# Optimization experiments

Hardware: AMD Instinct MI355X
Metric: run time of the kernel (lower is better)

Reference implementation:

```python
import jax, jax.numpy as jnp
import numpy as np

B, D, N, K = 4, 256, 4096, 8192


def setup_inputs() -> dict:
    key = jax.random.key(0)
    kx, ke = jax.random.split(key)
    x = jax.random.normal(kx, (B, D, N), dtype=jnp.float32)
    e = jax.random.normal(ke, (K, D), dtype=jnp.float32)
    return {"x": x, "e": e}


def reference(x, e):
    # encode: cdist(x^T [B,N,D], e [K,D]) -> [B,N,K]; argmin over K.
    # sqrt is monotonic, so argmin of squared distance == argmin of cdist.
    xt = jnp.transpose(x, (0, 2, 1))                      # [B,N,D]
    x2 = jnp.sum(xt * xt, axis=-1, keepdims=True)         # [B,N,1]
    e2 = jnp.sum(e * e, axis=-1)                          # [K]
    d2 = x2 - 2.0 * jnp.einsum('bnd,kd->bnk', xt, e) + e2 # [B,N,K]
    codes = jnp.argmin(d2, axis=-1)                       # [B,N]
    # decode: embedding gather then transpose back to [B,D,N]
    quantized = e[codes]                                  # [B,N,D]
    return jnp.transpose(quantized, (0, 2, 1))            # [B,D,N]
```

## Files before the change

kernel.cpp:

```cpp
#include <hip/hip_runtime.h>
#include <stdint.h>

#define B_ 4
#define D_ 256
#define N_ 4096
#define K_ 8192
#define Q_ (B_*N_)

#define KSPLIT_ 4
#define KSLICE_ (K_/KSPLIT_)
#define CHUNK_ 64
#define NCHUNK_ (KSLICE_/CHUNK_)
#define QTILE_ 256

typedef __attribute__((ext_vector_type(8))) short bf16x8;
typedef __attribute__((ext_vector_type(16))) float f32x16;

__device__ __forceinline__ unsigned short f32_to_bf16(float f) {
  unsigned u = __float_as_uint(f);
  unsigned r = 0x7FFFu + ((u >> 16) & 1u);
  return (unsigned short)((u + r) >> 16);
}
__device__ __forceinline__ float bf16_to_f32(unsigned short h) {
  return __uint_as_float(((unsigned)h) << 16);
}

__device__ __forceinline__ void gl_lds16(const void* g, void* l) {
  __builtin_amdgcn_global_load_lds(
      (const __attribute__((address_space(1))) unsigned int*)g,
      (__attribute__((address_space(3))) unsigned int*)l, 16, 0, 0);
}

__global__ void prep_x_kernel(const float* __restrict__ x,
                              unsigned short* __restrict__ xh,
                              unsigned short* __restrict__ xl) {
  __shared__ float tile[32][33];
  int b = blockIdx.z;
  int d0 = blockIdx.y * 32;
  int n0 = blockIdx.x * 32;
  int tx = threadIdx.x, ty = threadIdx.y;
  const float* xp = x + ((size_t)b * D_ + d0) * N_ + n0;
#pragma unroll
  for (int i = 0; i < 4; ++i)
    tile[ty + 8 * i][tx] = xp[(size_t)(ty + 8 * i) * N_ + tx];
  __syncthreads();
#pragma unroll
  for (int i = 0; i < 4; ++i) {
    int nl = ty + 8 * i;
    float v = -tile[tx][nl];
    unsigned short h = f32_to_bf16(v);
    unsigned short l = f32_to_bf16(v - bf16_to_f32(h));
    size_t q = (size_t)b * N_ + n0 + nl;
    xh[q * D_ + d0 + tx] = h;
    xl[q * D_ + d0 + tx] = l;
  }
}

__global__ void prep_e_kernel(const float* __restrict__ e,
                              unsigned short* __restrict__ eh,
                              unsigned short* __restrict__ el,
                              float* __restrict__ e2h,
                              unsigned long long* __restrict__ keys) {
  int k = blockIdx.x;
  int d = threadIdx.x;
  if (d < 2) keys[(size_t)k * 2 + d] = ~0ull;
  float v = e[(size_t)k * D_ + d];
  unsigned short h = f32_to_bf16(v);
  unsigned short l = f32_to_bf16(v - bf16_to_f32(h));
  eh[(size_t)k * D_ + d] = h;
  el[(size_t)k * D_ + d] = l;
  float s = v * v;
#pragma unroll
  for (int off = 32; off > 0; off >>= 1) s += __shfl_down(s, off, 64);
  __shared__ float ws4[4];
  if ((threadIdx.x & 63) == 0) ws4[threadIdx.x >> 6] = s;
  __syncthreads();
  if (threadIdx.x == 0) e2h[k] = 0.5f * (ws4[0] + ws4[1] + ws4[2] + ws4[3]);
}

__global__ __launch_bounds__(512, 2) void vq_main_kernel(
    const unsigned short* __restrict__ xh, const unsigned short* __restrict__ xl,
    const unsigned short* __restrict__ eh, const unsigned short* __restrict__ el,
    const float* __restrict__ e2h, unsigned long long* __restrict__ keys) {
  __shared__ __attribute__((aligned(16))) unsigned short Bs[2][2][CHUNK_ * 256];

  const int tid = threadIdx.x;
  const int w = tid >> 6;
  const int lane = tid & 63;
  const int l = lane & 31;
  const int hi = lane >> 5;

  const int qt = blockIdx.x >> 2;
  const int ksl = blockIdx.x & 3;
  const int q0 = qt * QTILE_;
  const int kbase = ksl * KSLICE_;
  const int qw = q0 + w * 32;

  bf16x8 ah[16], al[16];
  {
    const unsigned short* pa = xh + (size_t)(qw + l) * D_ + hi * 8;
    const unsigned short* pb = xl + (size_t)(qw + l) * D_ + hi * 8;
#pragma unroll
    for (int kc16 = 0; kc16 < 16; ++kc16) {
      ah[kc16] = *(const bf16x8*)(pa + kc16 * 16);
      al[kc16] = *(const bf16x8*)(pb + kc16 * 16);
    }
  }

  float rminv[16];
  int rmini[16];
#pragma unroll
  for (int r = 0; r < 16; ++r) { rminv[r] = __builtin_inff(); rmini[r] = 0; }

  auto stage = [&](int ch, int buf) {
    const int kc = kbase + ch * CHUNK_;
#pragma unroll
    for (int p = 0; p < 4; ++p) {
      const int c0 = w * 8 + p * 2;
      const int c = c0 + hi;
      const int g = l ^ (c & 31);
      const size_t srcoff = (size_t)(kc + c) * D_ + g * 8;
      gl_lds16(eh + srcoff, &Bs[buf][0][c0 * 256]);
      gl_lds16(el + srcoff, &Bs[buf][1][c0 * 256]);
    }
  };

  stage(0, 0);

#pragma unroll 1
  for (int ch = 0; ch < NCHUNK_; ++ch) {
    const int buf = ch & 1;
    __syncthreads();
    if (ch + 1 < NCHUNK_) stage(ch + 1, buf ^ 1);
    const int kc = kbase + ch * CHUNK_;
    const float e2v0 = e2h[kc + l];
    const float e2v1 = e2h[kc + 32 + l];

    {
      f32x16 acc;
#pragma unroll
      for (int r = 0; r < 16; ++r) acc[r] = e2v0;
#pragma unroll
      for (int ks = 0; ks < 16; ++ks) {
        const int pos = (((ks * 2 + hi) ^ l) * 8);
        bf16x8 bh = *(const bf16x8*)&Bs[buf][0][l * 256 + pos];
        bf16x8 bl = *(const bf16x8*)&Bs[buf][1][l * 256 + pos];
        acc = __builtin_amdgcn_mfma_f32_32x32x16_bf16(ah[ks], bh, acc, 0, 0, 0);
        acc = __builtin_amdgcn_mfma_f32_32x32x16_bf16(ah[ks], bl, acc, 0, 0, 0);
        acc = __builtin_amdgcn_mfma_f32_32x32x16_bf16(al[ks], bh, acc, 0, 0, 0);
      }
      const int kidx = kc + l;
#pragma unroll
      for (int r = 0; r < 16; ++r) {
        bool better = acc[r] < rminv[r];
        rminv[r] = better ? acc[r] : rminv[r];
        rmini[r] = better ? kidx : rmini[r];
      }
    }

    {
      f32x16 acc;
#pragma unroll
      for (int r = 0; r < 16; ++r) acc[r] = e2v1;
#pragma unroll
      for (int ks = 0; ks < 16; ++ks) {
        const int pos = (((ks * 2 + hi) ^ l) * 8);
        bf16x8 bh = *(const bf16x8*)&Bs[buf][0][(32 + l) * 256 + pos];
        bf16x8 bl = *(const bf16x8*)&Bs[buf][1][(32 + l) * 256 + pos];
        acc = __builtin_amdgcn_mfma_f32_32x32x16_bf16(ah[ks], bh, acc, 0, 0, 0);
        acc = __builtin_amdgcn_mfma_f32_32x32x16_bf16(ah[ks], bl, acc, 0, 0, 0);
        acc = __builtin_amdgcn_mfma_f32_32x32x16_bf16(al[ks], bh, acc, 0, 0, 0);
      }
      const int kidx = kc + 32 + l;
#pragma unroll
      for (int r = 0; r < 16; ++r) {
        bool better = acc[r] < rminv[r];
        rminv[r] = better ? acc[r] : rminv[r];
        rmini[r] = better ? kidx : rmini[r];
      }
    }
  }

#pragma unroll
  for (int r = 0; r < 16; ++r) {
    float bv = rminv[r];
    int bi = rmini[r];
#pragma unroll
    for (int xm = 1; xm <= 16; xm <<= 1) {
      float ov = __shfl_xor(bv, xm, 64);
      int oi = __shfl_xor(bi, xm, 64);
      if (ov < bv || (ov == bv && oi < bi)) { bv = ov; bi = oi; }
    }
    if (l == 0) {
      const int m = (r & 3) + 8 * (r >> 2) + 4 * hi;
      const int qq = qw + m;
      unsigned su = __float_as_uint(bv);
      su ^= (unsigned)(((int)su >> 31) | 0x80000000u);
      unsigned long long key = ((unsigned long long)su << 32) | (unsigned)bi;
      atomicMin(keys + qq, key);
    }
  }
}

__global__ void decode_kernel(const unsigned long long* __restrict__ keys,
                              const float* __restrict__ e,
                              float* __restrict__ out) {
  __shared__ float tile[32][33];
  __shared__ int codes[32];
  int b = blockIdx.y;
  int n0 = blockIdx.x * 32;
  int tx = threadIdx.x, ty = threadIdx.y;
  if (ty == 0)
    codes[tx] = (int)(keys[(size_t)b * N_ + n0 + tx] & 0xFFFFFFFFull);
  __syncthreads();
#pragma unroll 1
  for (int d0 = 0; d0 < D_; d0 += 32) {
#pragma unroll
    for (int i = 0; i < 4; ++i) {
      int nl = ty + 8 * i;
      tile[nl][tx] = e[(size_t)codes[nl] * D_ + d0 + tx];
    }
    __syncthreads();
#pragma unroll
    for (int i = 0; i < 4; ++i) {
      int dl = ty + 8 * i;
      out[((size_t)b * D_ + d0 + dl) * N_ + n0 + tx] = tile[tx][dl];
    }
    __syncthreads();
  }
}

extern "C" void kernel_launch(void* const* d_in, const int* in_sizes, int n_in,
                              void* d_out, int out_size, void* d_ws, size_t ws_size,
                              hipStream_t stream) {
  const float* x = (const float*)d_in[0];
  const float* e = (const float*)d_in[1];
  float* out = (float*)d_out;

  char* wksp = (char*)d_ws;
  unsigned short* xh = (unsigned short*)wksp;
  unsigned short* xl = xh + (size_t)Q_ * D_;
  unsigned short* eh = xl + (size_t)Q_ * D_;
  unsigned short* el = eh + (size_t)K_ * D_;
  float* e2h = (float*)(el + (size_t)K_ * D_);
  unsigned long long* keys = (unsigned long long*)(e2h + K_);

  prep_x_kernel<<<dim3(N_ / 32, D_ / 32, B_), dim3(32, 8), 0, stream>>>(x, xh, xl);
  prep_e_kernel<<<K_, 256, 0, stream>>>(e, eh, el, e2h, keys);
  vq_main_kernel<<<(Q_ / QTILE_) * KSPLIT_, 512, 0, stream>>>(xh, xl, eh, el, e2h, keys);
  decode_kernel<<<dim3(N_ / 32, B_), dim3(32, 8), 0, stream>>>(keys, e, out);
}
```

Measured before the change: 252.8 us.

## Pack argmin indices into bytes and software-pipeline LDS reads across two accumulators

The running argmin index per row is now stored as an 8-bit sub-chunk id packed four per register instead of a full int per row, freeing about 12 VGPRs. The two 32-column sub-chunks are merged into one 32-step loop with register double-buffered LDS reads two steps ahead, feeding two independent accumulators. The e2 term is applied at comparison time (e2 - acc) instead of seeding the accumulator, so x no longer needs negating in prep. This trades extra bit-manipulation ALU work for lower register pressure and better overlap of LDS latency with MFMA.

```diff
diff --git a/kernel.cpp b/kernel.cpp
--- a/kernel.cpp
+++ b/kernel.cpp
@@ -47,7 +47,7 @@
 #pragma unroll
   for (int i = 0; i < 4; ++i) {
     int nl = ty + 8 * i;
-    float v = -tile[tx][nl];
+    float v = tile[tx][nl];
     unsigned short h = f32_to_bf16(v);
     unsigned short l = f32_to_bf16(v - bf16_to_f32(h));
     size_t q = (size_t)b * N_ + n0 + nl;
@@ -108,9 +108,11 @@
   }
 
   float rminv[16];
-  int rmini[16];
-#pragma unroll
-  for (int r = 0; r < 16; ++r) { rminv[r] = __builtin_inff(); rmini[r] = 0; }
+  unsigned rmp[4];
+#pragma unroll
+  for (int r = 0; r < 16; ++r) rminv[r] = __builtin_inff();
+#pragma unroll
+  for (int i = 0; i < 4; ++i) rmp[i] = 0u;
 
   auto stage = [&](int ch, int buf) {
     const int kc = kbase + ch * CHUNK_;
@@ -136,47 +138,57 @@
     const float e2v0 = e2h[kc + l];
     const float e2v1 = e2h[kc + 32 + l];
 
+    const unsigned short* bh_base = &Bs[buf][0][0];
+    const unsigned short* bl_base = &Bs[buf][1][0];
+#define RD(base, kk) \
+    (*(const bf16x8*)&(base)[(((kk) >> 4) * 32 + l) * 256 + \
+                             (((((kk) & 15) * 2 + hi) ^ l) * 8)])
+
+    f32x16 acc0, acc1;
+#pragma unroll
+    for (int r = 0; r < 16; ++r) { acc0[r] = 0.f; acc1[r] = 0.f; }
+
+    bf16x8 cbh = RD(bh_base, 0), cbl = RD(bl_base, 0);
+    bf16x8 nbh = RD(bh_base, 1), nbl = RD(bl_base, 1);
+#pragma unroll
+    for (int kk = 0; kk < 32; ++kk) {
+      const bf16x8 ubh = cbh, ubl = cbl;
+      cbh = nbh; cbl = nbl;
+      if (kk + 2 < 32) { nbh = RD(bh_base, kk + 2); nbl = RD(bl_base, kk + 2); }
+      const int ks = kk & 15;
+      if (kk < 16) {
+        acc0 = __builtin_amdgcn_mfma_f32_32x32x16_bf16(ah[ks], ubh, acc0, 0, 0, 0);
+        acc0 = __builtin_amdgcn_mfma_f32_32x32x16_bf16(ah[ks], ubl, acc0, 0, 0, 0);
+        acc0 = __builtin_amdgcn_mfma_f32_32x32x16_bf16(al[ks], ubh, acc0, 0, 0, 0);
+      } else {
+        acc1 = __builtin_amdgcn_mfma_f32_32x32x16_bf16(ah[ks], ubh, acc1, 0, 0, 0);
+        acc1 = __builtin_amdgcn_mfma_f32_32x32x16_bf16(ah[ks], ubl, acc1, 0, 0, 0);
+        acc1 = __builtin_amdgcn_mfma_f32_32x32x16_bf16(al[ks], ubh, acc1, 0, 0, 0);
+      }
+      if (kk == 15) {
+        const unsigned vc = (unsigned)(ch * 2 + 0);
+#pragma unroll
+        for (int r = 0; r < 16; ++r) {
+          float dv = e2v0 - acc0[r];
+          bool better = dv < rminv[r];
+          rminv[r] = better ? dv : rminv[r];
+          const unsigned sh = (r & 3) * 8;
+          unsigned np = (rmp[r >> 2] & ~(0xFFu << sh)) | (vc << sh);
+          rmp[r >> 2] = better ? np : rmp[r >> 2];
+        }
+      }
+    }
+#undef RD
     {
-      f32x16 acc;
-#pragma unroll
-      for (int r = 0; r < 16; ++r) acc[r] = e2v0;
-#pragma unroll
-      for (int ks = 0; ks < 16; ++ks) {
-        const int pos = (((ks * 2 + hi) ^ l) * 8);
-        bf16x8 bh = *(const bf16x8*)&Bs[buf][0][l * 256 + pos];
-        bf16x8 bl = *(const bf16x8*)&Bs[buf][1][l * 256 + pos];
-        acc = __builtin_amdgcn_mfma_f32_32x32x16_bf16(ah[ks], bh, acc, 0, 0, 0);
-        acc = __builtin_amdgcn_mfma_f32_32x32x16_bf16(ah[ks], bl, acc, 0, 0, 0);
-        acc = __builtin_amdgcn_mfma_f32_32x32x16_bf16(al[ks], bh, acc, 0, 0, 0);
-      }
-      const int kidx = kc + l;
+      const unsigned vc = (unsigned)(ch * 2 + 1);
 #pragma unroll
       for (int r = 0; r < 16; ++r) {
-        bool better = acc[r] < rminv[r];
-        rminv[r] = better ? acc[r] : rminv[r];
-        rmini[r] = better ? kidx : rmini[r];
-      }
-    }
-
-    {
-      f32x16 acc;
-#pragma unroll
-      for (int r = 0; r < 16; ++r) acc[r] = e2v1;
-#pragma unroll
-      for (int ks = 0; ks < 16; ++ks) {
-        const int pos = (((ks * 2 + hi) ^ l) * 8);
-        bf16x8 bh = *(const bf16x8*)&Bs[buf][0][(32 + l) * 256 + pos];
-        bf16x8 bl = *(const bf16x8*)&Bs[buf][1][(32 + l) * 256 + pos];
-        acc = __builtin_amdgcn_mfma_f32_32x32x16_bf16(ah[ks], bh, acc, 0, 0, 0);
-        acc = __builtin_amdgcn_mfma_f32_32x32x16_bf16(ah[ks], bl, acc, 0, 0, 0);
-        acc = __builtin_amdgcn_mfma_f32_32x32x16_bf16(al[ks], bh, acc, 0, 0, 0);
-      }
-      const int kidx = kc + 32 + l;
-#pragma unroll
-      for (int r = 0; r < 16; ++r) {
-        bool better = acc[r] < rminv[r];
-        rminv[r] = better ? acc[r] : rminv[r];
-        rmini[r] = better ? kidx : rmini[r];
+        float dv = e2v1 - acc1[r];
+        bool better = dv < rminv[r];
+        rminv[r] = better ? dv : rminv[r];
+        const unsigned sh = (r & 3) * 8;
+        unsigned np = (rmp[r >> 2] & ~(0xFFu << sh)) | (vc << sh);
+        rmp[r >> 2] = better ? np : rmp[r >> 2];
       }
     }
   }
@@ -184,7 +196,8 @@
 #pragma unroll
   for (int r = 0; r < 16; ++r) {
     float bv = rminv[r];
-    int bi = rmini[r];
+    const unsigned sh = (r & 3) * 8;
+    int bi = kbase + (int)((rmp[r >> 2] >> sh) & 0xFFu) * 32 + l;
 #pragma unroll
     for (int xm = 1; xm <= 16; xm <<= 1) {
       float ov = __shfl_xor(bv, xm, 64);
```

After: 257.1 us. About the same (+1.7%).
